# Performance work log

Measured on AMD Instinct MI355X. Metric: run time of the kernel, lower is better.

## Reference

```python
import jax, jax.numpy as jnp
import numpy as np

B, N, DIM = 32, 576, 1024
H, HD = 16, 64            # head_dim = DIM // H
M = HD * 2                # rand_feat_dim = head_dim * rand_feat_dim_ratio(2) = 128
LAM = 0.1
NUM_STEP = 10
SCALE = HD ** (-0.5)


def setup_inputs() -> dict:
    key = jax.random.key(0)
    ks = jax.random.split(key, 6)
    x = jax.random.normal(ks[0], (B, N, DIM), dtype=jnp.float32)
    qkv_w = jax.random.normal(ks[1], (2 * DIM, DIM), dtype=jnp.float32) * 0.02
    proj_w = jax.random.normal(ks[2], (DIM, DIM), dtype=jnp.float32) * 0.02
    proj_b = jnp.zeros((DIM,), dtype=jnp.float32)
    rand_matrix = jax.random.normal(ks[3], (H, HD, M), dtype=jnp.float32)
    kernel = jax.random.normal(ks[4], (1, H, N, M), dtype=jnp.float32)
    learned_k = jnp.eye(2 * M, dtype=jnp.float32)
    learned_lam = jnp.ones((1,), dtype=jnp.float32)
    learned_L = jnp.ones((1,), dtype=jnp.float32)
    return {"x": x, "qkv_w": qkv_w, "proj_w": proj_w, "proj_b": proj_b,
            "rand_matrix": rand_matrix, "kernel": kernel,
            "learned_k": learned_k, "learned_lam": learned_lam,
            "learned_L": learned_L}


def _soft_thresh(z, t):
    # torch: sign(z) * GELU(|z| - t), exact (erf) GELU
    return jnp.sign(z) * jax.nn.gelu(jnp.abs(z) - t, approximate=False)


def reference(x, qkv_w, proj_w, proj_b, rand_matrix, kernel,
              learned_k, learned_lam, learned_L):
    # qkv projection (no bias), split into q and v heads: [B,H,N,HD]
    qkv = (x @ qkv_w.T).reshape(B, N, 2, H, HD)
    q = jnp.transpose(qkv[:, :, 0], (0, 2, 1, 3))
    v = jnp.transpose(qkv[:, :, 1], (0, 2, 1, 3))

    # random-feature map (Performer-style positive features)
    q = q * SCALE ** 0.5
    logits = jnp.einsum('bhnd,hdm->bhnm', q, rand_matrix)
    sqnorm = 0.5 * jnp.sum(q * q, axis=-1, keepdims=True)
    phi = jnp.exp(logits - sqnorm) / (M ** 0.5)                 # [B,H,N,M]

    # concat learned kernel features, L2-normalize over token dim (dim=-2)
    q = jnp.concatenate([phi, jnp.broadcast_to(kernel, (B, H, N, M))], axis=-1)
    nrm = jnp.linalg.norm(q, axis=-2, keepdims=True)
    q = q / jnp.maximum(nrm, 1e-12)                              # [B,H,N,2M]

    kk = jnp.einsum('bhnp,bhnq->bhpq', q, q)                     # [B,H,2M,2M]
    inp = jnp.einsum('bhnp,bhnd->bhpd', q, v)                    # [B,H,2M,HD]

    # ISTA-like unrolled solver
    L = jax.lax.stop_gradient(
        jnp.max(jnp.sum(jnp.abs(kk), axis=-1), axis=-1))[..., None, None] + 1.0
    lam_learned = learned_lam * LAM                              # [1]
    eff_L = L / learned_L                                        # [B,H,1,1]
    kk_learned = jnp.einsum('pq,bhqr,rs->bhps', learned_k, kk, learned_k)

    z = _soft_thresh(inp, lam_learned)
    for _ in range(NUM_STEP):
        z = z - (jnp.einsum('bhpq,bhqd->bhpd', kk_learned, z) - inp) / eff_L
        z = _soft_thresh(z, lam_learned / eff_L)

    out = jnp.einsum('bhnp,bhpd->bhnd', q, z)                    # [B,H,N,HD]
    out = jnp.transpose(out, (0, 2, 1, 3)).reshape(B, N, DIM)
    return out @ proj_w.T + proj_b
```

## Files before the change

### kernel.cpp

```cpp
#include <hip/hip_runtime.h>
#include <math.h>

#define NN 576
#define LAMC 0.1f
#define NUM_STEP 10

typedef unsigned short u16;
typedef __attribute__((ext_vector_type(8))) short bf16x8;
typedef __attribute__((ext_vector_type(4))) float f32x4;

__device__ __forceinline__ float bf2f(u16 u) { return __uint_as_float(((unsigned)u) << 16); }
__device__ __forceinline__ u16 f2bf(float f) {
    unsigned x = __float_as_uint(f);
    return (u16)((x + 0x7fffu + ((x >> 16) & 1u)) >> 16);
}
__device__ __forceinline__ float soft_thresh(float z, float t) {
    float a = fabsf(z) - t;
    float g = 0.5f * a * (1.0f + erff(a * 0.70710678118654752f));
    float s = (z > 0.0f) ? 1.0f : ((z < 0.0f) ? -1.0f : 0.0f);
    return s * g;
}
__device__ __forceinline__ void gload16(const u16* g, const u16* l) {
    __builtin_amdgcn_global_load_lds(
        (const __attribute__((address_space(1))) unsigned int*)(g),
        (__attribute__((address_space(3))) unsigned int*)(l), 16, 0, 0);
}

__global__ __launch_bounds__(256) void k_cvt(const float* __restrict__ in,
                                             u16* __restrict__ out, int n4) {
    const int i = blockIdx.x * 256 + threadIdx.x;
    if (i >= n4) return;
    float4 v = reinterpret_cast<const float4*>(in)[i];
    ushort4 o;
    o.x = f2bf(v.x); o.y = f2bf(v.y); o.z = f2bf(v.z); o.w = f2bf(v.w);
    reinterpret_cast<ushort4*>(out)[i] = o;
}

__global__ __launch_bounds__(256) void k_cvtT(const float* __restrict__ Lk,
                                              u16* __restrict__ LkT) {
    const int r = blockIdx.x, s = threadIdx.x;
    LkT[r * 256 + s] = f2bf(Lk[s * 256 + r]);
}

__global__ __launch_bounds__(256) void k_randT(const float* __restrict__ rand_m,
                                               u16* __restrict__ randT) {
    const int i = blockIdx.x * 256 + threadIdx.x;
    const int h = i >> 13, rem = i & 8191;
    const int m = rem >> 6, d = rem & 63;
    randT[i] = f2bf(rand_m[(size_t)h * 8192 + d * 128 + m]);
}

__device__ __forceinline__ void nt128_body(const u16* __restrict__ A, const u16* __restrict__ B,
                                           const int K, u16 (&As)[128][32], u16 (&Bs)[128][32],
                                           f32x4 (&acc)[4][4]) {
    const int tid = threadIdx.x;
    const int lane = tid & 63, wid = tid >> 6;
    const int wr = (wid >> 1) * 64, wc = (wid & 1) * 64;
    const int fr = lane & 15, kg = lane >> 4;
    for (int k0 = 0; k0 < K; k0 += 32) {
        __syncthreads();
        #pragma unroll
        for (int c = 0; c < 2; ++c) {
            const int ch = wid + c * 4;
            gload16(&A[(size_t)(ch * 16 + (lane >> 2)) * K + k0 + (lane & 3) * 8], &As[ch * 16][0]);
            gload16(&B[(size_t)(ch * 16 + (lane >> 2)) * K + k0 + (lane & 3) * 8], &Bs[ch * 16][0]);
        }
        __syncthreads();
        bf16x8 af[4], bfr[4];
        #pragma unroll
        for (int i = 0; i < 4; ++i) af[i] = *reinterpret_cast<const bf16x8*>(&As[wr + i * 16 + fr][kg * 8]);
        #pragma unroll
        for (int j = 0; j < 4; ++j) bfr[j] = *reinterpret_cast<const bf16x8*>(&Bs[wc + j * 16 + fr][kg * 8]);
        #pragma unroll
        for (int i = 0; i < 4; ++i)
            #pragma unroll
            for (int j = 0; j < 4; ++j)
                acc[i][j] = __builtin_amdgcn_mfma_f32_16x16x32_bf16(af[i], bfr[j], acc[i][j], 0, 0, 0);
    }
}

__device__ __forceinline__ void store_c_bf16(u16* __restrict__ C, f32x4 (&acc)[4][4]) {
    const int tid = threadIdx.x;
    const int lane = tid & 63, wid = tid >> 6;
    const int wr = (wid >> 1) * 64, wc = (wid & 1) * 64;
    const int fr = lane & 15, kg = lane >> 4;
    #pragma unroll
    for (int i = 0; i < 4; ++i)
        #pragma unroll
        for (int r = 0; r < 4; ++r)
            #pragma unroll
            for (int j = 0; j < 4; ++j)
                C[(size_t)(wr + i * 16 + kg * 4 + r) * 256 + wc + j * 16 + fr] = f2bf(acc[i][j][r]);
}

__global__ __launch_bounds__(256) void k_qkv_mfma(const u16* __restrict__ A,
                                                  const u16* __restrict__ B,
                                                  u16* __restrict__ qbf,
                                                  u16* __restrict__ vT) {
    __shared__ u16 As[128][32];
    __shared__ u16 Bs[128][32];
    const int tid = threadIdx.x;
    const int wid = tid >> 6, lane = tid & 63;
    const int wr = (wid >> 1) * 64, wc = (wid & 1) * 64;
    const int lb = (blockIdx.x & 7) * 288 + (blockIdx.x >> 3);
    const int bm = lb >> 4, bn = lb & 15;
    const int row0 = bm * 128, col0 = bn * 128;
    const int fr = lane & 15, kg = lane >> 4;
    f32x4 acc[4][4];
    #pragma unroll
    for (int i = 0; i < 4; ++i)
        #pragma unroll
        for (int j = 0; j < 4; ++j) acc[i][j] = (f32x4){0.f, 0.f, 0.f, 0.f};
    nt128_body(A + (size_t)row0 * 1024, B + (size_t)col0 * 1024, 1024, As, Bs, acc);
    const bool isQ = (col0 < 1024);
    if (isQ) {
        const float qscale = 0.35355339059327373f;
        #pragma unroll
        for (int i = 0; i < 4; ++i) {
            #pragma unroll
            for (int r = 0; r < 4; ++r) {
                const int grow = row0 + wr + i * 16 + kg * 4 + r;
                const int b = grow / NN, n = grow % NN;
                #pragma unroll
                for (int j = 0; j < 4; ++j) {
                    const int gcol = col0 + wc + j * 16 + fr;
                    const int h = gcol >> 6, d = gcol & 63;
                    qbf[(((size_t)b * 16 + h) * NN + n) * 64 + d] = f2bf(acc[i][j][r] * qscale);
                }
            }
        }
    } else {
        #pragma unroll
        for (int i = 0; i < 4; ++i) {
            const int gb = row0 + wr + i * 16 + kg * 4;
            const int b = gb / NN, n = gb % NN;
            #pragma unroll
            for (int j = 0; j < 4; ++j) {
                const int c2 = col0 + wc + j * 16 + fr - 1024;
                const int h = c2 >> 6, d = c2 & 63;
                ushort4 pk;
                pk.x = f2bf(acc[i][j][0]); pk.y = f2bf(acc[i][j][1]);
                pk.z = f2bf(acc[i][j][2]); pk.w = f2bf(acc[i][j][3]);
                *reinterpret_cast<ushort4*>(&vT[(((size_t)b * 16 + h) * 64 + d) * 576 + n]) = pk;
            }
        }
    }
}

__global__ __launch_bounds__(256) void k_phi_mfma(const u16* __restrict__ qbf,
                                                  const u16* __restrict__ randT,
                                                  u16* __restrict__ phiT,
                                                  float* __restrict__ invn) {
    __shared__ u16 Rs[128][72];
    __shared__ u16 Qs[64][72];
    __shared__ u16 Ph[128][72];
    __shared__ float sn[64];
    __shared__ float snorm[256];
    const int bh = blockIdx.x, h = bh & 15;
    const int tid = threadIdx.x, lane = tid & 63, wid = tid >> 6;
    const int fr = lane & 15, kg = lane >> 4;
    #pragma unroll
    for (int c = 0; c < 4; ++c) {
        const int i = c * 256 + tid;
        const int m = i >> 3, k8 = (i & 7) * 8;
        *reinterpret_cast<uint4*>(&Rs[m][k8]) =
            *reinterpret_cast<const uint4*>(&randT[((size_t)h * 128 + m) * 64 + k8]);
    }
    const u16* Q = qbf + (size_t)bh * 576 * 64;
    const float invM = 0.08838834764831845f;
    float accs = 0.f;
    const int m2 = tid >> 1, c0 = (tid & 1) * 32;
    for (int nc = 0; nc < 9; ++nc) {
        const int n0 = nc * 64;
        __syncthreads();
        #pragma unroll
        for (int c = 0; c < 2; ++c) {
            const int i = c * 256 + tid;
            const int r = i >> 3, k8 = (i & 7) * 8;
            *reinterpret_cast<uint4*>(&Qs[r][k8]) =
                *reinterpret_cast<const uint4*>(&Q[(size_t)(n0 + r) * 64 + k8]);
        }
        __syncthreads();
        if (tid < 64) {
            float s = 0.f;
            #pragma unroll 8
            for (int d = 0; d < 64; ++d) { float v = bf2f(Qs[tid][d]); s = fmaf(v, v, s); }
            sn[tid] = 0.5f * s;
        }
        f32x4 acc[2][4];
        #pragma unroll
        for (int i = 0; i < 2; ++i)
            #pragma unroll
            for (int j = 0; j < 4; ++j) acc[i][j] = (f32x4){0.f, 0.f, 0.f, 0.f};
        #pragma unroll
        for (int ks = 0; ks < 2; ++ks) {
            bf16x8 af[2], bq[4];
            #pragma unroll
            for (int i = 0; i < 2; ++i)
                af[i] = *reinterpret_cast<const bf16x8*>(&Rs[wid * 32 + i * 16 + fr][ks * 32 + kg * 8]);
            #pragma unroll
            for (int j = 0; j < 4; ++j)
                bq[j] = *reinterpret_cast<const bf16x8*>(&Qs[j * 16 + fr][ks * 32 + kg * 8]);
            #pragma unroll
            for (int i = 0; i < 2; ++i)
                #pragma unroll
                for (int j = 0; j < 4; ++j)
                    acc[i][j] = __builtin_amdgcn_mfma_f32_16x16x32_bf16(af[i], bq[j], acc[i][j], 0, 0, 0);
        }
        __syncthreads();
        #pragma unroll
        for (int j = 0; j < 4; ++j) {
            const int n = j * 16 + fr;
            const float sv = sn[n];
            #pragma unroll
            for (int i = 0; i < 2; ++i) {
                #pragma unroll
                for (int r = 0; r < 4; ++r) {
                    const int m = wid * 32 + i * 16 + kg * 4 + r;
                    Ph[m][n] = f2bf(expf(acc[i][j][r] - sv) * invM);
                }
            }
        }
        __syncthreads();
        #pragma unroll
        for (int c = 0; c < 4; ++c) {
            const int i = c * 256 + tid;
            const int mm = i >> 3, k8 = (i & 7) * 8;
            *reinterpret_cast<uint4*>(&phiT[((size_t)bh * 128 + mm) * 576 + n0 + k8]) =
                *reinterpret_cast<const uint4*>(&Ph[mm][k8]);
        }
        {
            float s = 0.f;
            #pragma unroll 8
            for (int t = 0; t < 32; ++t) { float v = bf2f(Ph[m2][c0 + t]); s = fmaf(v, v, s); }
            accs += s;
        }
    }
    snorm[tid] = accs;
    __syncthreads();
    if (tid < 128)
        invn[bh * 128 + tid] = 1.0f / fmaxf(sqrtf(snorm[tid * 2] + snorm[tid * 2 + 1]), 1e-12f);
}

__global__ __launch_bounds__(128) void k_kernormT(const float* __restrict__ kern,
                                                  u16* __restrict__ kerT) {
    const int h = blockIdx.x, m = threadIdx.x;
    const float* kp = kern + (size_t)h * NN * 128 + m;
    float s = 0.f;
    for (int n = 0; n < NN; ++n) { float v = kp[(size_t)n * 128]; s = fmaf(v, v, s); }
    const float inv = 1.0f / fmaxf(sqrtf(s), 1e-12f);
    u16* op = kerT + ((size_t)h * 128 + m) * 576;
    for (int n = 0; n < NN; ++n) op[n] = f2bf(kp[(size_t)n * 128] * inv);
}

__global__ __launch_bounds__(256) void k_gram_mfma(const u16* __restrict__ phiT,
                                                   const u16* __restrict__ kerT,
                                                   const float* __restrict__ invn,
                                                   u16* __restrict__ kkb) {
    __shared__ u16 As[128][32];
    __shared__ u16 Bs[128][32];
    const int lb = (blockIdx.x & 7) * 256 + (blockIdx.x >> 3);
    const int bh = lb >> 2, bm = (lb >> 1) & 1, bn = lb & 1;
    const int h = bh & 15;
    const u16* A = bm ? kerT + (size_t)h * 73728 : phiT + (size_t)bh * 73728;
    const u16* B = bn ? kerT + (size_t)h * 73728 : phiT + (size_t)bh * 73728;
    f32x4 acc[4][4];
    #pragma unroll
    for (int i = 0; i < 4; ++i)
        #pragma unroll
        for (int j = 0; j < 4; ++j) acc[i][j] = (f32x4){0.f, 0.f, 0.f, 0.f};
    nt128_body(A, B, 576, As, Bs, acc);
    const int tid = threadIdx.x, lane = tid & 63, wid = tid >> 6;
    const int wr = (wid >> 1) * 64, wc = (wid & 1) * 64;
    const int fr = lane & 15, kg = lane >> 4;
    const float* iv = invn + bh * 128;
    u16* C = kkb + (size_t)bh * 65536 + bm * 128 * 256 + bn * 128;
    float sq[4];
    #pragma unroll
    for (int j = 0; j < 4; ++j) sq[j] = bn ? 1.0f : iv[wc + j * 16 + fr];
    #pragma unroll
    for (int i = 0; i < 4; ++i)
        #pragma unroll
        for (int r = 0; r < 4; ++r) {
            const int p = wr + i * 16 + kg * 4 + r;
            const float sp = bm ? 1.0f : iv[p];
            #pragma unroll
            for (int j = 0; j < 4; ++j)
                C[(size_t)p * 256 + wc + j * 16 + fr] = f2bf(acc[i][j][r] * sp * sq[j]);
        }
}

__global__ __launch_bounds__(256) void k_lk_mfma(const u16* __restrict__ Ab, size_t sA,
                                                 const u16* __restrict__ Bb, size_t sB,
                                                 u16* __restrict__ Cb) {
    __shared__ u16 As[128][32];
    __shared__ u16 Bs[128][32];
    const int lb = (blockIdx.x & 7) * 256 + (blockIdx.x >> 3);
    const int idx = lb >> 2, bm = (lb >> 1) & 1, bn = lb & 1;
    const u16* A = Ab + (size_t)idx * sA + bm * 128 * 256;
    const u16* B = Bb + (size_t)idx * sB + bn * 128 * 256;
    f32x4 acc[4][4];
    #pragma unroll
    for (int i = 0; i < 4; ++i)
        #pragma unroll
        for (int j = 0; j < 4; ++j) acc[i][j] = (f32x4){0.f, 0.f, 0.f, 0.f};
    nt128_body(A, B, 256, As, Bs, acc);
    store_c_bf16(Cb + (size_t)idx * 65536 + bm * 128 * 256 + bn * 128, acc);
}

__global__ __launch_bounds__(256) void k_inp_mfma(const u16* __restrict__ vT,
                                                  const u16* __restrict__ phiT,
                                                  const u16* __restrict__ kerT,
                                                  const float* __restrict__ invn,
                                                  float* __restrict__ inpT) {
    __shared__ u16 As[64][40];
    __shared__ u16 Bs[256][40];
    const int bh = blockIdx.x, h = bh & 15;
    const int tid = threadIdx.x, lane = tid & 63, wid = tid >> 6;
    const int fr = lane & 15, kg = lane >> 4;
    const u16* Av = vT + (size_t)bh * 64 * 576;
    f32x4 acc[4][4];
    #pragma unroll
    for (int i = 0; i < 4; ++i)
        #pragma unroll
        for (int j = 0; j < 4; ++j) acc[i][j] = (f32x4){0.f, 0.f, 0.f, 0.f};
    for (int k0 = 0; k0 < 576; k0 += 32) {
        __syncthreads();
        { const int r = tid >> 2, k8 = (tid & 3) * 8;
          *reinterpret_cast<uint4*>(&As[r][k8]) =
              *reinterpret_cast<const uint4*>(&Av[(size_t)r * 576 + k0 + k8]); }
        #pragma unroll
        for (int c = 0; c < 4; ++c) {
            const int q = c * 256 + tid;
            const int r = q >> 2, k8 = (q & 3) * 8;
            const u16* src = (r < 128) ? phiT + ((size_t)bh * 128 + r) * 576
                                       : kerT + ((size_t)h * 128 + (r - 128)) * 576;
            *reinterpret_cast<uint4*>(&Bs[r][k8]) =
                *reinterpret_cast<const uint4*>(&src[k0 + k8]);
        }
        __syncthreads();
        bf16x8 af[4], bfr[4];
        #pragma unroll
        for (int i = 0; i < 4; ++i) af[i] = *reinterpret_cast<const bf16x8*>(&As[i * 16 + fr][kg * 8]);
        #pragma unroll
        for (int j = 0; j < 4; ++j) bfr[j] = *reinterpret_cast<const bf16x8*>(&Bs[wid * 64 + j * 16 + fr][kg * 8]);
        #pragma unroll
        for (int i = 0; i < 4; ++i)
            #pragma unroll
            for (int j = 0; j < 4; ++j)
                acc[i][j] = __builtin_amdgcn_mfma_f32_16x16x32_bf16(af[i], bfr[j], acc[i][j], 0, 0, 0);
    }
    float* O = inpT + (size_t)bh * 16384;
    float sc[4];
    #pragma unroll
    for (int j = 0; j < 4; ++j) {
        const int p = wid * 64 + j * 16 + fr;
        sc[j] = (p < 128) ? invn[bh * 128 + p] : 1.0f;
    }
    #pragma unroll
    for (int i = 0; i < 4; ++i)
        #pragma unroll
        for (int r = 0; r < 4; ++r)
            #pragma unroll
            for (int j = 0; j < 4; ++j)
                O[(size_t)(i * 16 + kg * 4 + r) * 256 + wid * 64 + j * 16 + fr] = acc[i][j][r] * sc[j];
}

__global__ __launch_bounds__(256) void k_L(const u16* __restrict__ kkb,
                                           const float* __restrict__ lL,
                                           float* __restrict__ effL) {
    const int bh = blockIdx.x;
    const u16* row = kkb + (size_t)bh * 65536 + (size_t)threadIdx.x * 256;
    float s = 0.f;
    for (int q = 0; q < 256; ++q) s += fabsf(bf2f(row[q]));
    __shared__ float red[256];
    red[threadIdx.x] = s;
    __syncthreads();
    for (int st = 128; st > 0; st >>= 1) {
        if (threadIdx.x < st) red[threadIdx.x] = fmaxf(red[threadIdx.x], red[threadIdx.x + st]);
        __syncthreads();
    }
    if (threadIdx.x == 0) effL[bh] = (red[0] + 1.0f) / lL[0];
}

__global__ __launch_bounds__(256) void k_ista_reg(const u16* __restrict__ kkl,
                                                  const float* __restrict__ inpT,
                                                  u16* __restrict__ zbf,
                                                  const float* __restrict__ effL,
                                                  const float* __restrict__ llam) {
    __shared__ u16 zs[32][256];
    const int bh = blockIdx.x >> 1, dh = blockIdx.x & 1;
    const int tid = threadIdx.x, lane = tid & 63, wid = tid >> 6;
    const int wr = wid * 64;
    const int fr = lane & 15, kg = lane >> 4;
    const u16* Kk = kkl + (size_t)bh * 65536;
    bf16x8 af[4][8];
    #pragma unroll
    for (int i = 0; i < 4; ++i) {
        const int p = wr + i * 16 + fr;
        #pragma unroll
        for (int c = 0; c < 8; ++c)
            af[i][c] = *reinterpret_cast<const bf16x8*>(&Kk[(size_t)p * 256 + c * 32 + kg * 8]);
    }
    const float* I = inpT + (size_t)bh * 16384 + (size_t)dh * 32 * 256;
    const float invL = 1.0f / effL[bh];
    const float lam = llam[0] * LAMC;
    const float thr = lam * invL;
    float4 ip[4][2];
    #pragma unroll
    for (int i = 0; i < 4; ++i) {
        const int pb = wr + i * 16 + kg * 4;
        #pragma unroll
        for (int j = 0; j < 2; ++j) {
            const int d = j * 16 + fr;
            ip[i][j] = *reinterpret_cast<const float4*>(&I[(size_t)d * 256 + pb]);
            const int pc = pb ^ ((d & 7) << 3);
            ushort4 pk;
            pk.x = f2bf(soft_thresh(ip[i][j].x, lam));
            pk.y = f2bf(soft_thresh(ip[i][j].y, lam));
            pk.z = f2bf(soft_thresh(ip[i][j].z, lam));
            pk.w = f2bf(soft_thresh(ip[i][j].w, lam));
            *reinterpret_cast<ushort4*>(&zs[d][pc]) = pk;
        }
    }
    __syncthreads();
    for (int step = 0; step < NUM_STEP; ++step) {
        f32x4 acc[4][2];
        #pragma unroll
        for (int i = 0; i < 4; ++i)
            #pragma unroll
            for (int j = 0; j < 2; ++j) acc[i][j] = (f32x4){0.f, 0.f, 0.f, 0.f};
        #pragma unroll
        for (int c = 0; c < 8; ++c) {
            bf16x8 bz[2];
            #pragma unroll
            for (int j = 0; j < 2; ++j) {
                const int d = j * 16 + fr;
                bz[j] = *reinterpret_cast<const bf16x8*>(&zs[d][(c * 32 + kg * 8) ^ ((d & 7) << 3)]);
            }
            #pragma unroll
            for (int i = 0; i < 4; ++i)
                #pragma unroll
                for (int j = 0; j < 2; ++j)
                    acc[i][j] = __builtin_amdgcn_mfma_f32_16x16x32_bf16(af[i][c], bz[j], acc[i][j], 0, 0, 0);
        }
        __syncthreads();
        #pragma unroll
        for (int i = 0; i < 4; ++i) {
            const int pb = wr + i * 16 + kg * 4;
            #pragma unroll
            for (int j = 0; j < 2; ++j) {
                const int d = j * 16 + fr;
                const int pc = pb ^ ((d & 7) << 3);
                ushort4 zo = *reinterpret_cast<const ushort4*>(&zs[d][pc]);
                ushort4 pk;
                pk.x = f2bf(soft_thresh(bf2f(zo.x) - (acc[i][j][0] - ip[i][j].x) * invL, thr));
                pk.y = f2bf(soft_thresh(bf2f(zo.y) - (acc[i][j][1] - ip[i][j].y) * invL, thr));
                pk.z = f2bf(soft_thresh(bf2f(zo.z) - (acc[i][j][2] - ip[i][j].z) * invL, thr));
                pk.w = f2bf(soft_thresh(bf2f(zo.w) - (acc[i][j][3] - ip[i][j].w) * invL, thr));
                *reinterpret_cast<ushort4*>(&zs[d][pc]) = pk;
            }
        }
        __syncthreads();
    }
    u16* Z = zbf + (size_t)bh * 16384 + (size_t)dh * 32 * 256;
    #pragma unroll
    for (int c = 0; c < 4; ++c) {
        const int i = c * 256 + tid;
        const int d = i >> 5, p8 = (i & 31) * 8;
        *reinterpret_cast<uint4*>(&Z[(size_t)d * 256 + p8]) =
            *reinterpret_cast<const uint4*>(&zs[d][p8 ^ ((d & 7) << 3)]);
    }
}

__global__ __launch_bounds__(256) void k_outpre_mfma(const u16* __restrict__ phiT,
                                                     const u16* __restrict__ kerT,
                                                     const u16* __restrict__ zbf,
                                                     const float* __restrict__ invn,
                                                     u16* __restrict__ outp) {
    __shared__ u16 Zs[64][264];
    __shared__ u16 Qt[64][264];
    __shared__ u16 Os[64][72];
    const int bh = blockIdx.x, b = bh >> 4, h = bh & 15;
    const int tid = threadIdx.x, lane = tid & 63, wid = tid >> 6;
    const int fr = lane & 15, kg = lane >> 4;
    const u16* Z = zbf + (size_t)bh * 16384;
    #pragma unroll
    for (int c = 0; c < 8; ++c) {
        const int i = c * 256 + tid;
        const int d = i >> 5, k8 = (i & 31) * 8;
        uint4 v = *reinterpret_cast<const uint4*>(&Z[(size_t)d * 256 + k8]);
        if (k8 < 128) {
            const float4 s0 = *reinterpret_cast<const float4*>(&invn[bh * 128 + k8]);
            const float4 s1 = *reinterpret_cast<const float4*>(&invn[bh * 128 + k8 + 4]);
            uint4 o;
            o.x = (unsigned)f2bf(__uint_as_float(v.x << 16) * s0.x) |
                  ((unsigned)f2bf(__uint_as_float(v.x & 0xffff0000u) * s0.y) << 16);
            o.y = (unsigned)f2bf(__uint_as_float(v.y << 16) * s0.z) |
                  ((unsigned)f2bf(__uint_as_float(v.y & 0xffff0000u) * s0.w) << 16);
            o.z = (unsigned)f2bf(__uint_as_float(v.z << 16) * s1.x) |
                  ((unsigned)f2bf(__uint_as_float(v.z & 0xffff0000u) * s1.y) << 16);
            o.w = (unsigned)f2bf(__uint_as_float(v.w << 16) * s1.z) |
                  ((unsigned)f2bf(__uint_as_float(v.w & 0xffff0000u) * s1.w) << 16);
            v = o;
        }
        *reinterpret_cast<uint4*>(&Zs[d][k8]) = v;
    }
    for (int nc = 0; nc < 9; ++nc) {
        const int n0 = nc * 64;
        __syncthreads();
        #pragma unroll
        for (int c = 0; c < 8; ++c) {
            const int i = c * 256 + tid;
            const int p = i >> 3, j8 = (i & 7) * 8;
            const u16* src = (p < 128) ? &phiT[((size_t)bh * 128 + p) * 576 + n0 + j8]
                                       : &kerT[((size_t)h * 128 + (p - 128)) * 576 + n0 + j8];
            uint4 v = *reinterpret_cast<const uint4*>(src);
            Qt[j8 + 0][p] = (u16)(v.x & 0xffffu); Qt[j8 + 1][p] = (u16)(v.x >> 16);
            Qt[j8 + 2][p] = (u16)(v.y & 0xffffu); Qt[j8 + 3][p] = (u16)(v.y >> 16);
            Qt[j8 + 4][p] = (u16)(v.z & 0xffffu); Qt[j8 + 5][p] = (u16)(v.z >> 16);
            Qt[j8 + 6][p] = (u16)(v.w & 0xffffu); Qt[j8 + 7][p] = (u16)(v.w >> 16);
        }
        __syncthreads();
        f32x4 acc[4];
        #pragma unroll
        for (int j = 0; j < 4; ++j) acc[j] = (f32x4){0.f, 0.f, 0.f, 0.f};
        #pragma unroll
        for (int ks = 0; ks < 8; ++ks) {
            bf16x8 aq = *reinterpret_cast<const bf16x8*>(&Qt[wid * 16 + fr][ks * 32 + kg * 8]);
            #pragma unroll
            for (int j = 0; j < 4; ++j) {
                bf16x8 bz = *reinterpret_cast<const bf16x8*>(&Zs[j * 16 + fr][ks * 32 + kg * 8]);
                acc[j] = __builtin_amdgcn_mfma_f32_16x16x32_bf16(aq, bz, acc[j], 0, 0, 0);
            }
        }
        __syncthreads();
        #pragma unroll
        for (int j = 0; j < 4; ++j)
            #pragma unroll
            for (int r = 0; r < 4; ++r)
                Os[wid * 16 + kg * 4 + r][j * 16 + fr] = f2bf(acc[j][r]);
        __syncthreads();
        #pragma unroll
        for (int c = 0; c < 2; ++c) {
            const int i = c * 256 + tid;
            const int nn = i >> 3, k8 = (i & 7) * 8;
            *reinterpret_cast<uint4*>(&outp[((size_t)b * NN + n0 + nn) * 1024 + h * 64 + k8]) =
                *reinterpret_cast<const uint4*>(&Os[nn][k8]);
        }
    }
}

__global__ __launch_bounds__(256) void k_proj_mfma(const u16* __restrict__ A,
                                                   const u16* __restrict__ B,
                                                   const float* __restrict__ bias,
                                                   float* __restrict__ out) {
    __shared__ u16 As[128][32];
    __shared__ u16 Bs[128][32];
    const int tid = threadIdx.x;
    const int wid = tid >> 6, lane = tid & 63;
    const int wr = (wid >> 1) * 64, wc = (wid & 1) * 64;
    const int lb = (blockIdx.x & 7) * 144 + (blockIdx.x >> 3);
    const int bm = lb >> 3, bn = lb & 7;
    const int row0 = bm * 128, col0 = bn * 128;
    const int fr = lane & 15, kg = lane >> 4;
    f32x4 acc[4][4];
    #pragma unroll
    for (int i = 0; i < 4; ++i)
        #pragma unroll
        for (int j = 0; j < 4; ++j) acc[i][j] = (f32x4){0.f, 0.f, 0.f, 0.f};
    nt128_body(A + (size_t)row0 * 1024, B + (size_t)col0 * 1024, 1024, As, Bs, acc);
    #pragma unroll
    for (int i = 0; i < 4; ++i)
        #pragma unroll
        for (int r = 0; r < 4; ++r) {
            const int grow = row0 + wr + i * 16 + kg * 4 + r;
            #pragma unroll
            for (int j = 0; j < 4; ++j) {
                const int gcol = col0 + wc + j * 16 + fr;
                out[(size_t)grow * 1024 + gcol] = acc[i][j][r] + bias[gcol];
            }
        }
}

extern "C" void kernel_launch(void* const* d_in, const int* in_sizes, int n_in,
                              void* d_out, int out_size, void* d_ws, size_t ws_size,
                              hipStream_t stream) {
    const float* x      = (const float*)d_in[0];
    const float* qkv_w  = (const float*)d_in[1];
    const float* proj_w = (const float*)d_in[2];
    const float* proj_b = (const float*)d_in[3];
    const float* rand_m = (const float*)d_in[4];
    const float* kern   = (const float*)d_in[5];
    const float* Lk     = (const float*)d_in[6];
    const float* llam   = (const float*)d_in[7];
    const float* lL     = (const float*)d_in[8];
    float* out = (float*)d_out;

    const size_t NEED = 248514560ull;
    if (ws_size < NEED) { hipMemsetAsync(d_out, 0, (size_t)out_size * 4, stream); return; }
    char* base = (char*)d_ws;
    u16*   pwb  = (u16*)  (base + 0);
    float* effL = (float*)(base + 2097152);
    u16*   Lkb  = (u16*)  (base + 2099200);
    u16*   LkTb = (u16*)  (base + 2230272);
    u16*   kerT = (u16*)  (base + 2361344);
    u16*   randT= (u16*)  (base + 4720640);
    u16*   phiT = (u16*)  (base + 4982784);
    u16*   kkb  = (u16*)  (base + 80480256);
    float* inpT = (float*)(base + 147589120);
    u16*   zbf  = (u16*)  (base + 181143552);
    float* invn = (float*)(base + 248252416);
    u16*   vT   = (u16*)  (base + 80480256);
    u16*   wb   = (u16*)  (base + 118228992);
    u16*   qbf  = (u16*)  (base + 147589120);
    u16*   xb   = (u16*)  (base + 197920768);
    u16*   tmpb = (u16*)  (base + 181143552);
    u16*   outp = (u16*)  (base + 80480256);

    k_cvt        <<<18432, 256, 0, stream>>>(x, xb, 4718592);
    k_cvt        <<<2048,  256, 0, stream>>>(qkv_w, wb, 524288);
    k_cvt        <<<1024,  256, 0, stream>>>(proj_w, pwb, 262144);
    k_cvt        <<<64,    256, 0, stream>>>(Lk, Lkb, 16384);
    k_cvtT       <<<256,   256, 0, stream>>>(Lk, LkTb);
    k_randT      <<<512,   256, 0, stream>>>(rand_m, randT);
    k_kernormT   <<<16,    128, 0, stream>>>(kern, kerT);
    k_qkv_mfma   <<<2304,  256, 0, stream>>>(xb, wb, qbf, vT);
    k_phi_mfma   <<<512,   256, 0, stream>>>(qbf, randT, phiT, invn);
    k_inp_mfma   <<<512,   256, 0, stream>>>(vT, phiT, kerT, invn, inpT);
    k_gram_mfma  <<<2048,  256, 0, stream>>>(phiT, kerT, invn, kkb);
    k_L          <<<512,   256, 0, stream>>>(kkb, lL, effL);
    k_lk_mfma    <<<2048,  256, 0, stream>>>(Lkb, 0, kkb, 65536, tmpb);
    k_lk_mfma    <<<2048,  256, 0, stream>>>(tmpb, 65536, LkTb, 0, kkb);
    k_ista_reg   <<<1024,  256, 0, stream>>>(kkb, inpT, zbf, effL, llam);
    k_outpre_mfma<<<512,   256, 0, stream>>>(phiT, kerT, zbf, invn, outp);
    k_proj_mfma  <<<1152,  256, 0, stream>>>(outp, pwb, proj_b, out);
}
```

Measured before the change: 626.3 us.

## Compute full 256x256 gram and learned-k products per block with swizzled LDS

Replaces the 2x2-tiled gram and learned-kernel matmul kernels with one 512-thread block per (batch,head) that computes the whole 256x256 output. In the gram kernel the concatenated q features are loaded once into a single LDS tile and shared as both operands, so the phi/kernel rows are no longer re-fetched by four separate blocks. An XOR swizzle on LDS slots is added to reduce bank conflicts. The cost is fewer blocks (512 instead of 2048) and higher register pressure from 32 accumulators per thread, which may lower occupancy.

```diff
diff --git a/kernel.cpp b/kernel.cpp
--- a/kernel.cpp
+++ b/kernel.cpp
@@ -77,20 +77,6 @@
             for (int j = 0; j < 4; ++j)
                 acc[i][j] = __builtin_amdgcn_mfma_f32_16x16x32_bf16(af[i], bfr[j], acc[i][j], 0, 0, 0);
     }
-}
-
-__device__ __forceinline__ void store_c_bf16(u16* __restrict__ C, f32x4 (&acc)[4][4]) {
-    const int tid = threadIdx.x;
-    const int lane = tid & 63, wid = tid >> 6;
-    const int wr = (wid >> 1) * 64, wc = (wid & 1) * 64;
-    const int fr = lane & 15, kg = lane >> 4;
-    #pragma unroll
-    for (int i = 0; i < 4; ++i)
-        #pragma unroll
-        for (int r = 0; r < 4; ++r)
-            #pragma unroll
-            for (int j = 0; j < 4; ++j)
-                C[(size_t)(wr + i * 16 + kg * 4 + r) * 256 + wc + j * 16 + fr] = f2bf(acc[i][j][r]);
 }
 
 __global__ __launch_bounds__(256) void k_qkv_mfma(const u16* __restrict__ A,
@@ -253,59 +239,113 @@
     for (int n = 0; n < NN; ++n) op[n] = f2bf(kp[(size_t)n * 128] * inv);
 }
 
-__global__ __launch_bounds__(256) void k_gram_mfma(const u16* __restrict__ phiT,
-                                                   const u16* __restrict__ kerT,
-                                                   const float* __restrict__ invn,
-                                                   u16* __restrict__ kkb) {
-    __shared__ u16 As[128][32];
-    __shared__ u16 Bs[128][32];
-    const int lb = (blockIdx.x & 7) * 256 + (blockIdx.x >> 3);
-    const int bh = lb >> 2, bm = (lb >> 1) & 1, bn = lb & 1;
-    const int h = bh & 15;
-    const u16* A = bm ? kerT + (size_t)h * 73728 : phiT + (size_t)bh * 73728;
-    const u16* B = bn ? kerT + (size_t)h * 73728 : phiT + (size_t)bh * 73728;
-    f32x4 acc[4][4];
-    #pragma unroll
-    for (int i = 0; i < 4; ++i)
-        #pragma unroll
-        for (int j = 0; j < 4; ++j) acc[i][j] = (f32x4){0.f, 0.f, 0.f, 0.f};
-    nt128_body(A, B, 576, As, Bs, acc);
+__global__ __launch_bounds__(512, 2) void k_gram_fat(const u16* __restrict__ phiT,
+                                                     const u16* __restrict__ kerT,
+                                                     const float* __restrict__ invn,
+                                                     u16* __restrict__ kkb) {
+    __shared__ u16 Qs[256][32];
+    const int bh = blockIdx.x, h = bh & 15;
     const int tid = threadIdx.x, lane = tid & 63, wid = tid >> 6;
-    const int wr = (wid >> 1) * 64, wc = (wid & 1) * 64;
-    const int fr = lane & 15, kg = lane >> 4;
+    const int wr = (wid & 3) * 64, wc = (wid >> 2) * 128;
+    const int fr = lane & 15, kg = lane >> 4;
+    const int lrow = lane >> 2;
+    const int lslot = (lane & 3) ^ ((lane >> 3) & 3);
+    f32x4 acc[4][8];
+    #pragma unroll
+    for (int i = 0; i < 4; ++i)
+        #pragma unroll
+        for (int j = 0; j < 8; ++j) acc[i][j] = (f32x4){0.f, 0.f, 0.f, 0.f};
+    const int rslot = (kg ^ ((fr >> 1) & 3)) * 8;
+    for (int k0 = 0; k0 < 576; k0 += 32) {
+        __syncthreads();
+        #pragma unroll
+        for (int c = 0; c < 2; ++c) {
+            const int chunk = wid * 2 + c;
+            const int p = chunk * 16 + lrow;
+            const u16* src = (p < 128)
+                ? phiT + ((size_t)bh * 128 + p) * 576 + k0 + lslot * 8
+                : kerT + ((size_t)h * 128 + (p - 128)) * 576 + k0 + lslot * 8;
+            gload16(src, &Qs[chunk * 16][0]);
+        }
+        __syncthreads();
+        bf16x8 af[4], bf[8];
+        #pragma unroll
+        for (int i = 0; i < 4; ++i) af[i] = *reinterpret_cast<const bf16x8*>(&Qs[wr + i * 16 + fr][rslot]);
+        #pragma unroll
+        for (int j = 0; j < 8; ++j) bf[j] = *reinterpret_cast<const bf16x8*>(&Qs[wc + j * 16 + fr][rslot]);
+        #pragma unroll
+        for (int i = 0; i < 4; ++i)
+            #pragma unroll
+            for (int j = 0; j < 8; ++j)
+                acc[i][j] = __builtin_amdgcn_mfma_f32_16x16x32_bf16(af[i], bf[j], acc[i][j], 0, 0, 0);
+    }
     const float* iv = invn + bh * 128;
-    u16* C = kkb + (size_t)bh * 65536 + bm * 128 * 256 + bn * 128;
-    float sq[4];
-    #pragma unroll
-    for (int j = 0; j < 4; ++j) sq[j] = bn ? 1.0f : iv[wc + j * 16 + fr];
-    #pragma unroll
-    for (int i = 0; i < 4; ++i)
-        #pragma unroll
-        for (int r = 0; r < 4; ++r) {
-            const int p = wr + i * 16 + kg * 4 + r;
-            const float sp = bm ? 1.0f : iv[p];
-            #pragma unroll
-            for (int j = 0; j < 4; ++j)
-                C[(size_t)p * 256 + wc + j * 16 + fr] = f2bf(acc[i][j][r] * sp * sq[j]);
-        }
-}
-
-__global__ __launch_bounds__(256) void k_lk_mfma(const u16* __restrict__ Ab, size_t sA,
-                                                 const u16* __restrict__ Bb, size_t sB,
-                                                 u16* __restrict__ Cb) {
-    __shared__ u16 As[128][32];
-    __shared__ u16 Bs[128][32];
-    const int lb = (blockIdx.x & 7) * 256 + (blockIdx.x >> 3);
-    const int idx = lb >> 2, bm = (lb >> 1) & 1, bn = lb & 1;
-    const u16* A = Ab + (size_t)idx * sA + bm * 128 * 256;
-    const u16* B = Bb + (size_t)idx * sB + bn * 128 * 256;
-    f32x4 acc[4][4];
-    #pragma unroll
-    for (int i = 0; i < 4; ++i)
-        #pragma unroll
-        for (int j = 0; j < 4; ++j) acc[i][j] = (f32x4){0.f, 0.f, 0.f, 0.f};
-    nt128_body(A, B, 256, As, Bs, acc);
-    store_c_bf16(Cb + (size_t)idx * 65536 + bm * 128 * 256 + bn * 128, acc);
+    u16* C = kkb + (size_t)bh * 65536;
+    float sq[8];
+    #pragma unroll
+    for (int j = 0; j < 8; ++j) { const int q = wc + j * 16 + fr; sq[j] = (q < 128) ? iv[q] : 1.0f; }
+    #pragma unroll
+    for (int i = 0; i < 4; ++i)
+        #pragma unroll
+        for (int rr = 0; rr < 4; ++rr) {
+            const int p = wr + i * 16 + kg * 4 + rr;
+            const float sp = (p < 128) ? iv[p] : 1.0f;
+            #pragma unroll
+            for (int j = 0; j < 8; ++j)
+                C[(size_t)p * 256 + wc + j * 16 + fr] = f2bf(acc[i][j][rr] * sp * sq[j]);
+        }
+}
+
+__global__ __launch_bounds__(512, 2) void k_lk_fat(const u16* __restrict__ Ab, size_t sA,
+                                                   const u16* __restrict__ Bb, size_t sB,
+                                                   u16* __restrict__ Cb) {
+    __shared__ u16 As[256][32];
+    __shared__ u16 Bs[256][32];
+    const int idx = blockIdx.x;
+    const int tid = threadIdx.x, lane = tid & 63, wid = tid >> 6;
+    const int wr = (wid & 3) * 64, wc = (wid >> 2) * 128;
+    const int fr = lane & 15, kg = lane >> 4;
+    const int lrow = lane >> 2;
+    const int lslot = (lane & 3) ^ ((lane >> 3) & 3);
+    const u16* A = Ab + (size_t)idx * sA;
+    const u16* B = Bb + (size_t)idx * sB;
+    f32x4 acc[4][8];
+    #pragma unroll
+    for (int i = 0; i < 4; ++i)
+        #pragma unroll
+        for (int j = 0; j < 8; ++j) acc[i][j] = (f32x4){0.f, 0.f, 0.f, 0.f};
+    const int rslot = (kg ^ ((fr >> 1) & 3)) * 8;
+    for (int k0 = 0; k0 < 256; k0 += 32) {
+        __syncthreads();
+        #pragma unroll
+        for (int c = 0; c < 2; ++c) {
+            const int chunk = wid * 2 + c;
+            const int p = chunk * 16 + lrow;
+            gload16(&A[(size_t)p * 256 + k0 + lslot * 8], &As[chunk * 16][0]);
+            gload16(&B[(size_t)p * 256 + k0 + lslot * 8], &Bs[chunk * 16][0]);
+        }
+        __syncthreads();
+        bf16x8 af[4], bf[8];
+        #pragma unroll
+        for (int i = 0; i < 4; ++i) af[i] = *reinterpret_cast<const bf16x8*>(&As[wr + i * 16 + fr][rslot]);
+        #pragma unroll
+        for (int j = 0; j < 8; ++j) bf[j] = *reinterpret_cast<const bf16x8*>(&Bs[wc + j * 16 + fr][rslot]);
+        #pragma unroll
+        for (int i = 0; i < 4; ++i)
+            #pragma unroll
+            for (int j = 0; j < 8; ++j)
+                acc[i][j] = __builtin_amdgcn_mfma_f32_16x16x32_bf16(af[i], bf[j], acc[i][j], 0, 0, 0);
+    }
+    u16* C = Cb + (size_t)idx * 65536;
+    #pragma unroll
+    for (int i = 0; i < 4; ++i)
+        #pragma unroll
+        for (int rr = 0; rr < 4; ++rr) {
+            const int p = wr + i * 16 + kg * 4 + rr;
+            #pragma unroll
+            for (int j = 0; j < 8; ++j)
+                C[(size_t)p * 256 + wc + j * 16 + fr] = f2bf(acc[i][j][rr]);
+        }
 }
 
 __global__ __launch_bounds__(256) void k_inp_mfma(const u16* __restrict__ vT,
@@ -628,10 +668,10 @@
     k_qkv_mfma   <<<2304,  256, 0, stream>>>(xb, wb, qbf, vT);
     k_phi_mfma   <<<512,   256, 0, stream>>>(qbf, randT, phiT, invn);
     k_inp_mfma   <<<512,   256, 0, stream>>>(vT, phiT, kerT, invn, inpT);
-    k_gram_mfma  <<<2048,  256, 0, stream>>>(phiT, kerT, invn, kkb);
+    k_gram_fat   <<<512,   512, 0, stream>>>(phiT, kerT, invn, kkb);
     k_L          <<<512,   256, 0, stream>>>(kkb, lL, effL);
-    k_lk_mfma    <<<2048,  256, 0, stream>>>(Lkb, 0, kkb, 65536, tmpb);
-    k_lk_mfma    <<<2048,  256, 0, stream>>>(tmpb, 65536, LkTb, 0, kkb);
+    k_lk_fat     <<<512,   512, 0, stream>>>(Lkb, 0, kkb, 65536, tmpb);
+    k_lk_fat     <<<512,   512, 0, stream>>>(tmpb, 65536, LkTb, 0, kkb);
     k_ista_reg   <<<1024,  256, 0, stream>>>(kkb, inpT, zbf, effL, llam);
     k_outpre_mfma<<<512,   256, 0, stream>>>(phiT, kerT, zbf, invn, outp);
     k_proj_mfma  <<<1152,  256, 0, stream>>>(outp, pwb, proj_b, out);
```

Result: faster. 610.0 us (-2.6%).
